# Optimization experiments

Hardware: AMD Instinct MI355X
Metric: run time of the kernel (lower is better)

The kernel has to match this reference:

```python
import jax, jax.numpy as jnp
import numpy as np

D_MODEL = 2048
N_HEADS = 16
D_HEAD = D_MODEL // N_HEADS
D_FF = 4 * D_MODEL
LN_EPS = 1e-5


def setup_inputs() -> dict:
    key = jax.random.key(0)
    ks = jax.random.split(key, 12)
    s = 1.0 / np.sqrt(D_MODEL)
    sf = 1.0 / np.sqrt(D_FF)
    return {
        "x": jax.random.normal(ks[0], (1, 2048, D_MODEL), dtype=jnp.float32),
        "ln1_g": jnp.ones((D_MODEL,), jnp.float32),
        "ln1_b": jnp.zeros((D_MODEL,), jnp.float32),
        # weights stored [in, out] (transpose of torch layout; equivalent under random init)
        "Wq": jax.random.normal(ks[1], (D_MODEL, D_MODEL), jnp.float32) * s,
        "Wk": jax.random.normal(ks[2], (D_MODEL, D_MODEL), jnp.float32) * s,
        "Wv": jax.random.normal(ks[3], (D_MODEL, D_MODEL), jnp.float32) * s,
        "Wp": jax.random.normal(ks[4], (D_MODEL, D_MODEL), jnp.float32) * s,
        "bp": jnp.zeros((D_MODEL,), jnp.float32),
        "ln2_g": jnp.ones((D_MODEL,), jnp.float32),
        "ln2_b": jnp.zeros((D_MODEL,), jnp.float32),
        "W1": jax.random.normal(ks[5], (D_MODEL, D_FF), jnp.float32) * s,
        "b1": jnp.zeros((D_FF,), jnp.float32),
        "W2": jax.random.normal(ks[6], (D_FF, D_MODEL), jnp.float32) * sf,
        "b2": jnp.zeros((D_MODEL,), jnp.float32),
    }


def _layer_norm(x, g, b):
    mu = jnp.mean(x, axis=-1, keepdims=True)
    var = jnp.mean(jnp.square(x - mu), axis=-1, keepdims=True)
    return (x - mu) * jax.lax.rsqrt(var + LN_EPS) * g + b


def _attention(h, Wq, Wk, Wv, Wp, bp):
    B, S, E = h.shape
    q = (h @ Wq).reshape(B, S, N_HEADS, D_HEAD)
    k = (h @ Wk).reshape(B, S, N_HEADS, D_HEAD)
    v = (h @ Wv).reshape(B, S, N_HEADS, D_HEAD)
    # [B, H, S, S] causal scores (matches the naive materialized original)
    scores = jnp.einsum("bqhd,bkhd->bhqk", q, k) / np.sqrt(D_HEAD).astype(np.float32)
    causal = jnp.arange(S)[:, None] >= jnp.arange(S)[None, :]
    scores = jnp.where(causal, scores, -jnp.inf)
    attn = jax.nn.softmax(scores, axis=-1)
    out = jnp.einsum("bhqk,bkhd->bqhd", attn, v).reshape(B, S, E)
    return out @ Wp + bp


def reference(x, ln1_g, ln1_b, Wq, Wk, Wv, Wp, bp, ln2_g, ln2_b, W1, b1, W2, b2):
    # attention branch: x += MHA(LN1(x)); dropout=0 (inference)
    x1 = x + _attention(_layer_norm(x, ln1_g, ln1_b), Wq, Wk, Wv, Wp, bp)
    # ff branch: FeedForward adds its own residual on the normalized input
    g = _layer_norm(x1, ln2_g, ln2_b)
    mlp = jax.nn.gelu(g @ W1 + b1, approximate=False) @ W2 + b2
    return x1 + (g + mlp)
```

## Files before the change

### kernel.cpp

```cpp
#include <hip/hip_runtime.h>
#include <math.h>

typedef unsigned int u32;
typedef unsigned short u16;
typedef __attribute__((ext_vector_type(8))) short short8;
typedef __attribute__((ext_vector_type(4))) float f32x4;

__device__ __forceinline__ u16 f2bf(float f) {
  u32 u = __builtin_bit_cast(u32, f);
  u += 0x7FFFu + ((u >> 16) & 1u);
  return (u16)(u >> 16);
}
__device__ __forceinline__ float bf2f(u16 h) {
  u32 u = ((u32)h) << 16;
  return __builtin_bit_cast(float, u);
}
__device__ __forceinline__ void gload_lds16(const void* g, void* l) {
  __builtin_amdgcn_global_load_lds((const __attribute__((address_space(1))) u32*)g,
                                   (__attribute__((address_space(3))) u32*)l, 16, 0, 0);
}
__device__ __forceinline__ f32x4 mfma16(short8 a, short8 b, f32x4 c) {
  return __builtin_amdgcn_mfma_f32_16x16x32_bf16(a, b, c, 0, 0, 0);
}

__global__ __launch_bounds__(256) void transpose_cast(const float* __restrict__ src,
                                                      u16* __restrict__ dst, int K, int N) {
  __shared__ __attribute__((aligned(16))) u16 tile[64][72];
  const int n0 = blockIdx.x * 64, k0 = blockIdx.y * 64;
  const int t = threadIdx.x;
  const int tr = t >> 4;
  const int tc4 = (t & 15) * 4;
#pragma unroll
  for (int p = 0; p < 4; ++p) {
    int row = p * 16 + tr;
    const float4 v = *(const float4*)(src + (size_t)(k0 + row) * N + n0 + tc4);
    tile[tc4 + 0][row] = f2bf(v.x);
    tile[tc4 + 1][row] = f2bf(v.y);
    tile[tc4 + 2][row] = f2bf(v.z);
    tile[tc4 + 3][row] = f2bf(v.w);
  }
  __syncthreads();
  const int nr = t >> 2;
  const int kc = (t & 3) * 16;
  u16* d = dst + (size_t)(n0 + nr) * K + k0 + kc;
  *(short8*)(d) = *(const short8*)&tile[nr][kc];
  *(short8*)(d + 8) = *(const short8*)&tile[nr][kc + 8];
}

__global__ __launch_bounds__(256) void transpose_v(const u16* __restrict__ qkv,
                                                   u16* __restrict__ vT) {
  __shared__ __attribute__((aligned(16))) u16 tile[64][72];
  const int kv0 = blockIdx.x * 64, d0 = blockIdx.y * 64, h = blockIdx.z;
  const int t = threadIdx.x;
  const int tr = t >> 3;
  const int tc8 = (t & 7) * 8;
#pragma unroll
  for (int p = 0; p < 2; ++p) {
    int row = p * 32 + tr;
    short8 v = *(const short8*)(qkv + (size_t)(kv0 + row) * 6144 + 4096 + h * 128 + d0 + tc8);
#pragma unroll
    for (int j = 0; j < 8; ++j) tile[tc8 + j][row] = (u16)v[j];
  }
  __syncthreads();
  const int dr = t >> 2;
  const int kc = (t & 3) * 16;
  u16* dst = vT + ((size_t)h * 128 + d0 + dr) * 2048 + kv0 + kc;
  *(short8*)dst = *(const short8*)&tile[dr][kc];
  *(short8*)(dst + 8) = *(const short8*)&tile[dr][kc + 8];
}

__global__ __launch_bounds__(256) void ln_kernel(const float* __restrict__ x,
                                                 const float* __restrict__ gw,
                                                 const float* __restrict__ bw,
                                                 u16* __restrict__ out) {
  const int row = blockIdx.x, t = threadIdx.x;
  const float* xr = x + (size_t)row * 2048;
  const float4 v0 = *(const float4*)(xr + t * 8);
  const float4 v1 = *(const float4*)(xr + t * 8 + 4);
  float s = v0.x + v0.y + v0.z + v0.w + v1.x + v1.y + v1.z + v1.w;
  float q = v0.x * v0.x + v0.y * v0.y + v0.z * v0.z + v0.w * v0.w +
            v1.x * v1.x + v1.y * v1.y + v1.z * v1.z + v1.w * v1.w;
#pragma unroll
  for (int w = 32; w; w >>= 1) { s += __shfl_xor(s, w); q += __shfl_xor(q, w); }
  __shared__ float rs[4], rq[4];
  const int wid = t >> 6, lane = t & 63;
  if (!lane) { rs[wid] = s; rq[wid] = q; }
  __syncthreads();
  s = rs[0] + rs[1] + rs[2] + rs[3];
  q = rq[0] + rq[1] + rq[2] + rq[3];
  const float mu = s * (1.f / 2048.f);
  const float var = q * (1.f / 2048.f) - mu * mu;
  const float rstd = rsqrtf(var + 1e-5f);
  const float4 g0 = *(const float4*)(gw + t * 8);
  const float4 g1 = *(const float4*)(gw + t * 8 + 4);
  const float4 b0 = *(const float4*)(bw + t * 8);
  const float4 b1 = *(const float4*)(bw + t * 8 + 4);
  short8 o;
  o[0] = (short)f2bf((v0.x - mu) * rstd * g0.x + b0.x);
  o[1] = (short)f2bf((v0.y - mu) * rstd * g0.y + b0.y);
  o[2] = (short)f2bf((v0.z - mu) * rstd * g0.z + b0.z);
  o[3] = (short)f2bf((v0.w - mu) * rstd * g0.w + b0.w);
  o[4] = (short)f2bf((v1.x - mu) * rstd * g1.x + b1.x);
  o[5] = (short)f2bf((v1.y - mu) * rstd * g1.y + b1.y);
  o[6] = (short)f2bf((v1.z - mu) * rstd * g1.z + b1.z);
  o[7] = (short)f2bf((v1.w - mu) * rstd * g1.w + b1.w);
  *(short8*)(out + (size_t)row * 2048 + t * 8) = o;
}

template <int EPI>
__global__ __launch_bounds__(512, 2) void gemm3(const u16* __restrict__ A,
                                                const u16* __restrict__ Bt,
                                                int M, int N, int K, int Kc,
                                                u16* __restrict__ outB,
                                                const float* __restrict__ bias,
                                                float* __restrict__ pA,
                                                float* __restrict__ pB) {
  __shared__ __attribute__((aligned(16))) u16 lds[3 * 16384];
  const int m0 = blockIdx.y * 256, n0 = blockIdx.x * 256;
  const int tid = threadIdx.x, wid = tid >> 6, lane = tid & 63;
  const int wr = wid >> 2, wc = wid & 3;
  const int lq = lane & 15, lk = lane >> 4;
  const int kStart = blockIdx.z * Kc;
  const int NT = Kc / 32;

  size_t aoff[2], boff[2];
#pragma unroll
  for (int s = 0; s < 2; ++s) {
    int c = s * 512 + tid;
    int row = c >> 2;
    int col = ((c & 3) ^ ((row >> 1) & 3)) * 8;
    aoff[s] = (size_t)(m0 + row) * K + kStart + col;
    boff[s] = (size_t)(n0 + row) * K + kStart + col;
  }
  u16* ldst = lds + tid * 8;

#define STA(s, buf, t2) gload_lds16(A + aoff[s] + (size_t)((t2) * 32), \
                                    ldst + (buf) * 16384 + (s) * 4096)
#define STB(s, buf, t2) gload_lds16(Bt + boff[s] + (size_t)((t2) * 32), \
                                    ldst + (buf) * 16384 + 8192 + (s) * 4096)

  STA(0, 0, 0); STA(1, 0, 0); STB(0, 0, 0); STB(1, 0, 0);
  STA(0, 1, 1); STA(1, 1, 1); STB(0, 1, 1); STB(1, 1, 1);
  asm volatile("s_waitcnt vmcnt(4)" ::: "memory");
  __builtin_amdgcn_s_barrier();
  __builtin_amdgcn_sched_barrier(0);

  f32x4 acc[8][4] = {};
  int cur = 0, nxt2 = 2;
  for (int t = 0; t < NT; ++t) {
    const char* bufc = (const char*)lds + cur * 32768;
    const bool st = (t + 2) < NT;
    short8 bf[4], af[4];
#pragma unroll
    for (int ni = 0; ni < 4; ++ni) {
      int br = wc * 64 + ni * 16 + lq;
      bf[ni] = *(const short8*)(bufc + 16384 + br * 64 + ((lk ^ ((br >> 1) & 3)) << 4));
    }
#pragma unroll
    for (int mi = 0; mi < 4; ++mi) {
      int ar = wr * 128 + mi * 16 + lq;
      af[mi] = *(const short8*)(bufc + ar * 64 + ((lk ^ ((ar >> 1) & 3)) << 4));
    }
    if (st) { STA(0, nxt2, t + 2); STA(1, nxt2, t + 2); }
    __builtin_amdgcn_s_setprio(1);
#pragma unroll
    for (int mi = 0; mi < 4; ++mi)
#pragma unroll
      for (int ni = 0; ni < 4; ++ni)
        acc[mi][ni] = mfma16(af[mi], bf[ni], acc[mi][ni]);
    __builtin_amdgcn_s_setprio(0);
#pragma unroll
    for (int mi = 0; mi < 4; ++mi) {
      int ar = wr * 128 + (mi + 4) * 16 + lq;
      af[mi] = *(const short8*)(bufc + ar * 64 + ((lk ^ ((ar >> 1) & 3)) << 4));
    }
    if (st) { STB(0, nxt2, t + 2); STB(1, nxt2, t + 2); }
    __builtin_amdgcn_s_setprio(1);
#pragma unroll
    for (int mi = 0; mi < 4; ++mi)
#pragma unroll
      for (int ni = 0; ni < 4; ++ni)
        acc[mi + 4][ni] = mfma16(af[mi], bf[ni], acc[mi + 4][ni]);
    __builtin_amdgcn_s_setprio(0);
    if (st) asm volatile("s_waitcnt vmcnt(4)" ::: "memory");
    else    asm volatile("s_waitcnt vmcnt(0)" ::: "memory");
    __builtin_amdgcn_s_barrier();
    __builtin_amdgcn_sched_barrier(0);
    cur = (cur == 2) ? 0 : cur + 1;
    nxt2 = (nxt2 == 2) ? 0 : nxt2 + 1;
  }
#undef STA
#undef STB

  float* pp = nullptr;
  if (EPI == 4) {
    pp = (blockIdx.z < 2 ? pA : pB) + (size_t)(blockIdx.z & 1) * ((size_t)M * N);
  }
#pragma unroll
  for (int mi = 0; mi < 8; ++mi) {
#pragma unroll
    for (int ni = 0; ni < 4; ++ni) {
      const int col = n0 + wc * 64 + ni * 16 + lq;
#pragma unroll
      for (int r = 0; r < 4; ++r) {
        const int row = m0 + wr * 128 + mi * 16 + lk * 4 + r;
        const size_t idx = (size_t)row * N + col;
        float v = acc[mi][ni][r];
        if (EPI == 0) {
          outB[idx] = f2bf(v);
        } else if (EPI == 2) {
          float xg = v + bias[col];
          outB[idx] = f2bf(0.5f * xg * (1.f + erff(xg * 0.70710678118654752f)));
        } else {
          pp[idx] = v;
        }
      }
    }
  }
}

template <int NS, int RES2>
__global__ __launch_bounds__(256) void reduce_kernel(const float* __restrict__ pA,
                                                     const float* __restrict__ pB,
                                                     const float* __restrict__ bias,
                                                     const float* __restrict__ res1,
                                                     const u16* __restrict__ res2,
                                                     float* __restrict__ out,
                                                     int MN, int N) {
  const int i = (blockIdx.x * 256 + threadIdx.x) * 4;
  if (i >= MN) return;
  float4 s = *(const float4*)(pA + i);
  {
    const float4 t = *(const float4*)(pA + MN + i);
    s.x += t.x; s.y += t.y; s.z += t.z; s.w += t.w;
  }
  if (NS == 4) {
    const float4 t0 = *(const float4*)(pB + i);
    const float4 t1 = *(const float4*)(pB + MN + i);
    s.x += t0.x + t1.x; s.y += t0.y + t1.y; s.z += t0.z + t1.z; s.w += t0.w + t1.w;
  }
  const int col = i & (N - 1);
  const float4 bv = *(const float4*)(bias + col);
  const float4 r1 = *(const float4*)(res1 + i);
  float4 o;
  o.x = s.x + bv.x + r1.x;
  o.y = s.y + bv.y + r1.y;
  o.z = s.z + bv.z + r1.z;
  o.w = s.w + bv.w + r1.w;
  if (RES2) {
    const u16* r2 = res2 + i;
    o.x += bf2f(r2[0]); o.y += bf2f(r2[1]); o.z += bf2f(r2[2]); o.w += bf2f(r2[3]);
  }
  *(float4*)(out + i) = o;
}

__global__ __launch_bounds__(256) void attn_kernel(const u16* __restrict__ qkv,
                                                   const u16* __restrict__ vT,
                                                   u16* __restrict__ attnout) {
  __shared__ __attribute__((aligned(16))) u16 lsK[64 * 128];
  __shared__ __attribute__((aligned(16))) u16 lsV[128 * 64];
  __shared__ __attribute__((aligned(16))) u16 lsP[4][16 * 64];
  const int h = blockIdx.x;
  const int qi = 31 - blockIdx.y;
  const int qb = qi * 64;
  const int tid = threadIdx.x, wid = tid >> 6, lane = tid & 63;
  const int lq = lane & 15, lk = lane >> 4;
  const int qw = qb + wid * 16;

  short8 qf[4];
  {
    const u16* qp = qkv + (size_t)(qw + lq) * 6144 + h * 128;
#pragma unroll
    for (int ks = 0; ks < 4; ++ks) qf[ks] = *(const short8*)(qp + ks * 32 + lk * 8);
  }
  float mreg[4], lreg[4];
  f32x4 o[8];
#pragma unroll
  for (int r = 0; r < 4; ++r) { mreg[r] = -INFINITY; lreg[r] = 0.f; }
#pragma unroll
  for (int dt = 0; dt < 8; ++dt) o[dt] = (f32x4){0.f, 0.f, 0.f, 0.f};

  const int rK = lane >> 4, sK = lane & 15;
  const int rV = lane >> 3, sV = lane & 7;
  const int nkt = qi + 1;
  for (int kt = 0; kt < nkt; ++kt) {
    const int kv0 = kt * 64;
    if (kt) __syncthreads();
#pragma unroll
    for (int i = 0; i < 4; ++i) {
      int c = wid * 4 + i;
      int rowK = c * 4 + rK;
      gload_lds16(qkv + (size_t)(kv0 + rowK) * 6144 + 2048 + h * 128 + ((sK ^ (rowK & 7)) * 8),
                  lsK + c * 512);
      int rowV = c * 8 + rV;
      gload_lds16(vT + ((size_t)h * 128 + rowV) * 2048 + kv0 + ((sV ^ (rowV & 7)) * 8),
                  lsV + c * 512);
    }
    __syncthreads();

    f32x4 sc[4];
#pragma unroll
    for (int nt = 0; nt < 4; ++nt) sc[nt] = (f32x4){0.f, 0.f, 0.f, 0.f};
#pragma unroll
    for (int ks = 0; ks < 4; ++ks) {
#pragma unroll
      for (int nt = 0; nt < 4; ++nt) {
        int kvr = nt * 16 + lq;
        short8 kf = *(const short8*)((const char*)lsK + kvr * 256 +
                                     ((ks * 64 + lk * 16) ^ ((kvr & 7) << 4)));
        sc[nt] = mfma16(qf[ks], kf, sc[nt]);
      }
    }
    float rmax[4] = {-INFINITY, -INFINITY, -INFINITY, -INFINITY};
#pragma unroll
    for (int nt = 0; nt < 4; ++nt) {
      int kv = kv0 + nt * 16 + lq;
#pragma unroll
      for (int r = 0; r < 4; ++r) {
        int qrow = qw + lk * 4 + r;
        float s = (kv <= qrow) ? sc[nt][r] * 0.08838834764831845f : -INFINITY;
        sc[nt][r] = s;
        rmax[r] = fmaxf(rmax[r], s);
      }
    }
#pragma unroll
    for (int r = 0; r < 4; ++r)
#pragma unroll
      for (int w = 1; w < 16; w <<= 1) rmax[r] = fmaxf(rmax[r], __shfl_xor(rmax[r], w));
    bool grow = false;
#pragma unroll
    for (int r = 0; r < 4; ++r) grow |= (rmax[r] > mreg[r] + 8.f);
    if (__any(grow)) {
#pragma unroll
      for (int r = 0; r < 4; ++r) {
        float mn = fmaxf(mreg[r], rmax[r]);
        float alpha = __expf(mreg[r] - mn);
        mreg[r] = mn;
        lreg[r] *= alpha;
#pragma unroll
        for (int dt = 0; dt < 8; ++dt) o[dt][r] *= alpha;
      }
    }
    float rsum[4] = {0.f, 0.f, 0.f, 0.f};
    u16* P = &lsP[wid][0];
#pragma unroll
    for (int nt = 0; nt < 4; ++nt) {
#pragma unroll
      for (int r = 0; r < 4; ++r) {
        float p = __expf(sc[nt][r] - mreg[r]);
        rsum[r] += p;
        int prow = lk * 4 + r, pcol = nt * 16 + lq;
        *(u16*)((char*)P + prow * 128 + ((pcol * 2) ^ ((prow & 7) << 4))) = f2bf(p);
      }
    }
#pragma unroll
    for (int r = 0; r < 4; ++r) {
#pragma unroll
      for (int w = 1; w < 16; w <<= 1) rsum[r] += __shfl_xor(rsum[r], w);
      lreg[r] += rsum[r];
    }
#pragma unroll
    for (int kk = 0; kk < 2; ++kk) {
      short8 pa = *(const short8*)((const char*)P + lq * 128 +
                                   ((kk * 64 + lk * 16) ^ ((lq & 7) << 4)));
#pragma unroll
      for (int dt = 0; dt < 8; ++dt) {
        int dr = dt * 16 + lq;
        short8 vf = *(const short8*)((const char*)lsV + dr * 128 +
                                     ((kk * 64 + lk * 16) ^ ((dr & 7) << 4)));
        o[dt] = mfma16(pa, vf, o[dt]);
      }
    }
  }
#pragma unroll
  for (int r = 0; r < 4; ++r) {
    float inv = 1.f / lreg[r];
    int row = qw + lk * 4 + r;
    u16* op = attnout + (size_t)row * 2048 + h * 128 + lq;
#pragma unroll
    for (int dt = 0; dt < 8; ++dt) op[dt * 16] = f2bf(o[dt][r] * inv);
  }
}

extern "C" void kernel_launch(void* const* d_in, const int* in_sizes, int n_in,
                              void* d_out, int out_size, void* d_ws, size_t ws_size,
                              hipStream_t stream) {
  (void)in_sizes; (void)n_in; (void)out_size; (void)ws_size;
  const float* x    = (const float*)d_in[0];
  const float* ln1g = (const float*)d_in[1];
  const float* ln1b = (const float*)d_in[2];
  const float* Wq   = (const float*)d_in[3];
  const float* Wk   = (const float*)d_in[4];
  const float* Wv   = (const float*)d_in[5];
  const float* Wp   = (const float*)d_in[6];
  const float* bp   = (const float*)d_in[7];
  const float* ln2g = (const float*)d_in[8];
  const float* ln2b = (const float*)d_in[9];
  const float* W1   = (const float*)d_in[10];
  const float* b1   = (const float*)d_in[11];
  const float* W2   = (const float*)d_in[12];
  const float* b2   = (const float*)d_in[13];
  float* out = (float*)d_out;
  char* ws = (char*)d_ws;

  u16* wqkvT = (u16*)(ws + 0);
  u16* hbuf  = (u16*)(ws + 25165824);
  u16* wpT   = (u16*)(ws + 33554432);
  u16* w1T   = (u16*)(ws + 41943040);
  u16* w2T   = (u16*)(ws + 75497472);
  u16* qkv   = (u16*)(ws + 109051904);
  u16* vT    = (u16*)(ws + 134217728);
  u16* attn  = (u16*)(ws + 142606336);
  float* x1  = (float*)(ws + 150994944);
  u16* g     = (u16*)(ws + 167772160);
  u16* ff1   = (u16*)(ws + 0);
  float* projPA = (float*)(ws + 0);
  float* projPB = (float*)(ws + 109051904);
  float* ffPA = (float*)(ws + 33554432);
  float* ffPB = (float*)(ws + 109051904);

  dim3 b256(256), b512(512);
  transpose_cast<<<dim3(32, 32), b256, 0, stream>>>(Wq, wqkvT, 2048, 2048);
  transpose_cast<<<dim3(32, 32), b256, 0, stream>>>(Wk, wqkvT + 2048 * 2048, 2048, 2048);
  transpose_cast<<<dim3(32, 32), b256, 0, stream>>>(Wv, wqkvT + 4096 * 2048, 2048, 2048);
  transpose_cast<<<dim3(32, 32), b256, 0, stream>>>(Wp, wpT, 2048, 2048);
  transpose_cast<<<dim3(128, 32), b256, 0, stream>>>(W1, w1T, 2048, 8192);
  transpose_cast<<<dim3(32, 128), b256, 0, stream>>>(W2, w2T, 8192, 2048);
  ln_kernel<<<2048, b256, 0, stream>>>(x, ln1g, ln1b, hbuf);
  gemm3<0><<<dim3(24, 8, 1), b512, 0, stream>>>(hbuf, wqkvT, 2048, 6144, 2048, 2048,
                                                qkv, nullptr, nullptr, nullptr);
  transpose_v<<<dim3(32, 2, 16), b256, 0, stream>>>(qkv, vT);
  attn_kernel<<<dim3(16, 32), b256, 0, stream>>>(qkv, vT, attn);
  gemm3<4><<<dim3(8, 8, 4), b512, 0, stream>>>(attn, wpT, 2048, 2048, 2048, 512,
                                               nullptr, nullptr, projPA, projPB);
  reduce_kernel<4, 0><<<4096, b256, 0, stream>>>(projPA, projPB, bp, x, nullptr, x1,
                                                 4194304, 2048);
  ln_kernel<<<2048, b256, 0, stream>>>(x1, ln2g, ln2b, g);
  gemm3<2><<<dim3(32, 8, 1), b512, 0, stream>>>(g, w1T, 2048, 8192, 2048, 2048,
                                                ff1, b1, nullptr, nullptr);
  gemm3<4><<<dim3(8, 8, 4), b512, 0, stream>>>(ff1, w2T, 2048, 2048, 8192, 2048,
                                               nullptr, nullptr, ffPA, ffPB);
  reduce_kernel<4, 1><<<4096, b256, 0, stream>>>(ffPA, ffPB, b2, x1, g, out,
                                                 4194304, 2048);
}
```

Baseline: 423.8 us.

## Double-buffer attention K/V loads, fuse reduce with LN2, batch weight casts

Three changes. First, the four square weight transpose-casts are merged into a single launch with a z-dimension. Second, the split-K partial-sum reduction for the output projection is fused with the second layernorm, so x1 is not re-read and one launch is removed. Third, the attention kernel double-buffers its K/V tiles in LDS, issuing the next tile's global-to-LDS loads before computing the current one. This hides load latency at the cost of doubled LDS use, which may lower occupancy.

```diff
diff --git a/kernel.cpp b/kernel.cpp
--- a/kernel.cpp
+++ b/kernel.cpp
@@ -21,6 +21,37 @@
 }
 __device__ __forceinline__ f32x4 mfma16(short8 a, short8 b, f32x4 c) {
   return __builtin_amdgcn_mfma_f32_16x16x32_bf16(a, b, c, 0, 0, 0);
+}
+
+__global__ __launch_bounds__(256) void transpose_cast4(const float* __restrict__ Wq,
+                                                       const float* __restrict__ Wk,
+                                                       const float* __restrict__ Wv,
+                                                       const float* __restrict__ Wp,
+                                                       u16* __restrict__ wqkvT,
+                                                       u16* __restrict__ wpT) {
+  __shared__ __attribute__((aligned(16))) u16 tile[64][72];
+  const int z = blockIdx.z;
+  const float* src = (z == 0) ? Wq : (z == 1) ? Wk : (z == 2) ? Wv : Wp;
+  u16* dst = (z < 3) ? (wqkvT + (size_t)z * 2048 * 2048) : wpT;
+  const int n0 = blockIdx.x * 64, k0 = blockIdx.y * 64;
+  const int t = threadIdx.x;
+  const int tr = t >> 4;
+  const int tc4 = (t & 15) * 4;
+#pragma unroll
+  for (int p = 0; p < 4; ++p) {
+    int row = p * 16 + tr;
+    const float4 v = *(const float4*)(src + (size_t)(k0 + row) * 2048 + n0 + tc4);
+    tile[tc4 + 0][row] = f2bf(v.x);
+    tile[tc4 + 1][row] = f2bf(v.y);
+    tile[tc4 + 2][row] = f2bf(v.z);
+    tile[tc4 + 3][row] = f2bf(v.w);
+  }
+  __syncthreads();
+  const int nr = t >> 2;
+  const int kc = (t & 3) * 16;
+  u16* d = dst + (size_t)(n0 + nr) * 2048 + k0 + kc;
+  *(short8*)(d) = *(const short8*)&tile[nr][kc];
+  *(short8*)(d + 8) = *(const short8*)&tile[nr][kc + 8];
 }
 
 __global__ __launch_bounds__(256) void transpose_cast(const float* __restrict__ src,
@@ -107,6 +138,58 @@
   *(short8*)(out + (size_t)row * 2048 + t * 8) = o;
 }
 
+__global__ __launch_bounds__(256) void reduce_ln(const float* __restrict__ pA,
+                                                 const float* __restrict__ pB,
+                                                 const float* __restrict__ bias,
+                                                 const float* __restrict__ res1,
+                                                 const float* __restrict__ gw,
+                                                 const float* __restrict__ bw,
+                                                 float* __restrict__ x1,
+                                                 u16* __restrict__ g) {
+  const int row = blockIdx.x, t = threadIdx.x;
+  const size_t MN = 4194304;
+  const size_t base = (size_t)row * 2048 + t * 8;
+  float v[8];
+#pragma unroll
+  for (int half = 0; half < 2; ++half) {
+    float4 a0 = *(const float4*)(pA + base + half * 4);
+    float4 a1 = *(const float4*)(pA + MN + base + half * 4);
+    float4 b0 = *(const float4*)(pB + base + half * 4);
+    float4 b1 = *(const float4*)(pB + MN + base + half * 4);
+    float4 bi = *(const float4*)(bias + t * 8 + half * 4);
+    float4 r1 = *(const float4*)(res1 + base + half * 4);
+    v[half * 4 + 0] = a0.x + a1.x + b0.x + b1.x + bi.x + r1.x;
+    v[half * 4 + 1] = a0.y + a1.y + b0.y + b1.y + bi.y + r1.y;
+    v[half * 4 + 2] = a0.z + a1.z + b0.z + b1.z + bi.z + r1.z;
+    v[half * 4 + 3] = a0.w + a1.w + b0.w + b1.w + bi.w + r1.w;
+  }
+  float4 o0 = {v[0], v[1], v[2], v[3]}, o1 = {v[4], v[5], v[6], v[7]};
+  *(float4*)(x1 + base) = o0;
+  *(float4*)(x1 + base + 4) = o1;
+  float s = 0.f, q = 0.f;
+#pragma unroll
+  for (int j = 0; j < 8; ++j) { s += v[j]; q += v[j] * v[j]; }
+#pragma unroll
+  for (int w = 32; w; w >>= 1) { s += __shfl_xor(s, w); q += __shfl_xor(q, w); }
+  __shared__ float rs[4], rq[4];
+  const int wid = t >> 6, lane = t & 63;
+  if (!lane) { rs[wid] = s; rq[wid] = q; }
+  __syncthreads();
+  s = rs[0] + rs[1] + rs[2] + rs[3];
+  q = rq[0] + rq[1] + rq[2] + rq[3];
+  const float mu = s * (1.f / 2048.f);
+  const float var = q * (1.f / 2048.f) - mu * mu;
+  const float rstd = rsqrtf(var + 1e-5f);
+  short8 o;
+#pragma unroll
+  for (int j = 0; j < 8; ++j) {
+    float gj = *(gw + t * 8 + j);
+    float bj = *(bw + t * 8 + j);
+    o[j] = (short)f2bf((v[j] - mu) * rstd * gj + bj);
+  }
+  *(short8*)(g + base) = o;
+}
+
 template <int EPI>
 __global__ __launch_bounds__(512, 2) void gemm3(const u16* __restrict__ A,
                                                 const u16* __restrict__ Bt,
@@ -257,8 +340,8 @@
 __global__ __launch_bounds__(256) void attn_kernel(const u16* __restrict__ qkv,
                                                    const u16* __restrict__ vT,
                                                    u16* __restrict__ attnout) {
-  __shared__ __attribute__((aligned(16))) u16 lsK[64 * 128];
-  __shared__ __attribute__((aligned(16))) u16 lsV[128 * 64];
+  __shared__ __attribute__((aligned(16))) u16 lsK[2 * 64 * 128];
+  __shared__ __attribute__((aligned(16))) u16 lsV[2 * 128 * 64];
   __shared__ __attribute__((aligned(16))) u16 lsP[4][16 * 64];
   const int h = blockIdx.x;
   const int qi = 31 - blockIdx.y;
@@ -283,20 +366,35 @@
   const int rK = lane >> 4, sK = lane & 15;
   const int rV = lane >> 3, sV = lane & 7;
   const int nkt = qi + 1;
-  for (int kt = 0; kt < nkt; ++kt) {
-    const int kv0 = kt * 64;
-    if (kt) __syncthreads();
+
+  auto STAGE = [&](int kt_, int b_) {
+    const int kv0_ = kt_ * 64;
 #pragma unroll
     for (int i = 0; i < 4; ++i) {
       int c = wid * 4 + i;
       int rowK = c * 4 + rK;
-      gload_lds16(qkv + (size_t)(kv0 + rowK) * 6144 + 2048 + h * 128 + ((sK ^ (rowK & 7)) * 8),
-                  lsK + c * 512);
+      gload_lds16(qkv + (size_t)(kv0_ + rowK) * 6144 + 2048 + h * 128 + ((sK ^ (rowK & 7)) * 8),
+                  lsK + b_ * 8192 + c * 512);
       int rowV = c * 8 + rV;
-      gload_lds16(vT + ((size_t)h * 128 + rowV) * 2048 + kv0 + ((sV ^ (rowV & 7)) * 8),
-                  lsV + c * 512);
-    }
-    __syncthreads();
+      gload_lds16(vT + ((size_t)h * 128 + rowV) * 2048 + kv0_ + ((sV ^ (rowV & 7)) * 8),
+                  lsV + b_ * 8192 + c * 512);
+    }
+  };
+
+  STAGE(0, 0);
+  for (int kt = 0; kt < nkt; ++kt) {
+    const int b = kt & 1;
+    const int kv0 = kt * 64;
+    if (kt + 1 < nkt) {
+      STAGE(kt + 1, b ^ 1);
+      asm volatile("s_waitcnt vmcnt(8)" ::: "memory");
+    } else {
+      asm volatile("s_waitcnt vmcnt(0)" ::: "memory");
+    }
+    __builtin_amdgcn_s_barrier();
+    __builtin_amdgcn_sched_barrier(0);
+    const char* Kb = (const char*)(lsK + b * 8192);
+    const char* Vb = (const char*)(lsV + b * 8192);
 
     f32x4 sc[4];
 #pragma unroll
@@ -306,7 +404,7 @@
 #pragma unroll
       for (int nt = 0; nt < 4; ++nt) {
         int kvr = nt * 16 + lq;
-        short8 kf = *(const short8*)((const char*)lsK + kvr * 256 +
+        short8 kf = *(const short8*)(Kb + kvr * 256 +
                                      ((ks * 64 + lk * 16) ^ ((kvr & 7) << 4)));
         sc[nt] = mfma16(qf[ks], kf, sc[nt]);
       }
@@ -366,11 +464,12 @@
 #pragma unroll
       for (int dt = 0; dt < 8; ++dt) {
         int dr = dt * 16 + lq;
-        short8 vf = *(const short8*)((const char*)lsV + dr * 128 +
+        short8 vf = *(const short8*)(Vb + dr * 128 +
                                      ((kk * 64 + lk * 16) ^ ((dr & 7) << 4)));
         o[dt] = mfma16(pa, vf, o[dt]);
       }
     }
+    __builtin_amdgcn_s_barrier();
   }
 #pragma unroll
   for (int r = 0; r < 4; ++r) {
@@ -420,10 +519,7 @@
   float* ffPB = (float*)(ws + 109051904);
 
   dim3 b256(256), b512(512);
-  transpose_cast<<<dim3(32, 32), b256, 0, stream>>>(Wq, wqkvT, 2048, 2048);
-  transpose_cast<<<dim3(32, 32), b256, 0, stream>>>(Wk, wqkvT + 2048 * 2048, 2048, 2048);
-  transpose_cast<<<dim3(32, 32), b256, 0, stream>>>(Wv, wqkvT + 4096 * 2048, 2048, 2048);
-  transpose_cast<<<dim3(32, 32), b256, 0, stream>>>(Wp, wpT, 2048, 2048);
+  transpose_cast4<<<dim3(32, 32, 4), b256, 0, stream>>>(Wq, Wk, Wv, Wp, wqkvT, wpT);
   transpose_cast<<<dim3(128, 32), b256, 0, stream>>>(W1, w1T, 2048, 8192);
   transpose_cast<<<dim3(32, 128), b256, 0, stream>>>(W2, w2T, 8192, 2048);
   ln_kernel<<<2048, b256, 0, stream>>>(x, ln1g, ln1b, hbuf);
@@ -433,9 +529,7 @@
   attn_kernel<<<dim3(16, 32), b256, 0, stream>>>(qkv, vT, attn);
   gemm3<4><<<dim3(8, 8, 4), b512, 0, stream>>>(attn, wpT, 2048, 2048, 2048, 512,
                                                nullptr, nullptr, projPA, projPB);
-  reduce_kernel<4, 0><<<4096, b256, 0, stream>>>(projPA, projPB, bp, x, nullptr, x1,
-                                                 4194304, 2048);
-  ln_kernel<<<2048, b256, 0, stream>>>(x1, ln2g, ln2b, g);
+  reduce_ln<<<2048, b256, 0, stream>>>(projPA, projPB, bp, x, ln2g, ln2b, x1, g);
   gemm3<2><<<dim3(32, 8, 1), b512, 0, stream>>>(g, w1T, 2048, 8192, 2048, 2048,
                                                 ff1, b1, nullptr, nullptr);
   gemm3<4><<<dim3(8, 8, 4), b512, 0, stream>>>(ff1, w2T, 2048, 2048, 8192, 2048,
```

New measurement: 413.2 us. 2.5% less time.
